# Kernel optimization log

Measured on AMD Instinct MI355X. Metric: run time of the kernel, lower is better.

The kernel has to match this reference:

```python
import jax, jax.numpy as jnp
import numpy as np

N = 8000      # genes (nodes)
P = 32        # pathways (subgraphs, each over all N nodes)
E = 128000    # global edges
ES = 4096     # edges per pathway subgraph
DIN = 16      # in_dim (omics features)
D = 128       # in_dim * 8
K1, K2, K3 = 6400, 5120, 4096  # ceil(0.8*N), ceil(0.8*K1), ceil(0.8*K2)


def setup_inputs() -> dict:
    key = jax.random.key(0)
    ks = jax.random.split(key, 16)
    f = lambda i, shape: jax.random.normal(ks[i], shape, jnp.float32) * 0.05
    edge_index = jax.random.randint(ks[0], (2, E), 0, N, dtype=jnp.int32)
    base = jax.random.randint(ks[1], (2, P, ES), 0, N, dtype=jnp.int32)
    sub_edge_index = (base + (jnp.arange(P, dtype=jnp.int32) * N)[None, :, None]).reshape(2, -1)
    return dict(
        h=jax.random.normal(ks[2], (N, DIN), jnp.float32),
        edge_index=edge_index,
        sub_edge_index=sub_edge_index,
        Wl_a=f(3, (DIN, D)), Wr_a=f(4, (DIN, D)), bl_a=jnp.zeros((D,), jnp.float32),
        # stacked SAGEConv params: [0]=conv_b [1]=conv_c [2]=conv1 [3]=conv2 [4]=conv3
        Wl_s=f(5, (5, D, D)), Wr_s=f(6, (5, D, D)), bl_s=jnp.zeros((5, D), jnp.float32),
        # GlobalAttention gates: [0..2]=readout_a/b/c  [3..5]=readout1/2/3
        gate_w=f(7, (6, D)), gate_b=jnp.zeros((6,), jnp.float32),
        # SAGPooling score GraphConv (D->1): lin_rel (w,b) + lin_root (w)
        pool_wrel=f(8, (3, D)), pool_brel=jnp.zeros((3,), jnp.float32), pool_wroot=f(9, (3, D)),
        norm_w=jnp.ones((D,), jnp.float32), norm_b=jnp.zeros((D,), jnp.float32), norm_ms=jnp.ones((D,), jnp.float32),
        lin_w=f(10, (3 * D, 1)), lin_b=jnp.zeros((1,), jnp.float32),
        m1_w=f(11, (P + 1, 48)), m1_b=jnp.zeros((48,), jnp.float32),
        m2_w=f(12, (48, 16)), m2_b=jnp.zeros((16,), jnp.float32),
        m3_w=f(13, (16, 1)), m3_b=jnp.zeros((1,), jnp.float32),
    )


def _sage(x, src, dst, w, Wl, Wr, bl, n):
    # PyG SAGEConv (aggr='mean'): lin_l(mean_j x_j) + lin_r(x); w = edge live mask
    s = jax.ops.segment_sum(x[src] * w[:, None], dst, num_segments=n)
    deg = jax.ops.segment_sum(w, dst, num_segments=n)
    return (s / jnp.maximum(deg, 1.0)[:, None]) @ Wl + bl + x @ Wr


def _gnorm(x, w, b, ms):
    # PyG GraphNorm, single graph (batch=None)
    mu = x.mean(0)
    o = x - mu * ms
    var = (o * o).mean(0)
    return w * o / jnp.sqrt(var + 1e-5) + b


def reference(h, edge_index, sub_edge_index, Wl_a, Wr_a, bl_a, Wl_s, Wr_s, bl_s,
              gate_w, gate_b, pool_wrel, pool_brel, pool_wroot,
              norm_w, norm_b, norm_ms, lin_w, lin_b,
              m1_w, m1_b, m2_w, m2_b, m3_w, m3_b):
    # ---- stage 1: whole graph, add self loops ----
    loop = jnp.arange(N, dtype=edge_index.dtype)
    src = jnp.concatenate([edge_index[0], loop])
    dst = jnp.concatenate([edge_index[1], loop])
    w1 = jnp.ones(src.shape[0], h.dtype)

    def ro_single(x, i):  # GlobalAttention, batch=None -> one graph
        a = jax.nn.softmax(x @ gate_w[i] + gate_b[i])
        return (a @ x)[None, :]

    x = jnp.tanh(_sage(h, src, dst, w1, Wl_a, Wr_a, bl_a, N))
    x1 = ro_single(x, 0)
    x = _gnorm(x, norm_w, norm_b, norm_ms)
    x = jnp.tanh(_sage(x, src, dst, w1, Wl_s[0], Wr_s[0], bl_s[0], N))
    x2 = ro_single(x, 1)
    x = _gnorm(x, norm_w, norm_b, norm_ms)
    x = jnp.tanh(_sage(x, src, dst, w1, Wl_s[1], Wr_s[1], bl_s[1], N))
    x3 = ro_single(x, 2)
    readout1 = jnp.concatenate([x1, x2, x3], axis=1)  # [1, 3D]

    # ---- stage 2: P pathway subgraphs, each over all N nodes (Data(x=x, edge_index=sub)) ----
    X = jnp.tile(x, (P, 1))            # [P*N, D]
    ssrc, sdst = sub_edge_index[0], sub_edge_index[1]
    ealive = jnp.ones(ssrc.shape, bool)
    nalive = jnp.ones((P, N), bool)

    def sagpool(x, ealive, nalive, i, k):
        # score via GraphConv (aggr='add'); keep top-k per graph; x *= tanh(score)
        w = ealive.astype(x.dtype)
        agg = jax.ops.segment_sum(x[ssrc] * w[:, None], sdst, num_segments=P * N)
        score = agg @ pool_wrel[i] + pool_brel[i] + x @ pool_wroot[i]  # [P*N]
        masked = jnp.where(nalive, score.reshape(P, N), -jnp.inf)
        _, idx = jax.lax.top_k(masked, k)
        na = jnp.zeros((P, N), bool).at[jnp.arange(P)[:, None], idx].set(True)
        xm = jnp.where(na.reshape(-1, 1), x * jnp.tanh(score)[:, None], 0.0)
        naf = na.reshape(-1)
        return xm, ealive & naf[ssrc] & naf[sdst], na

    def ro_batch(x, nalive, i):  # GlobalAttention with batch vector (masked per-graph softmax)
        g = jnp.where(nalive, (x @ gate_w[i] + gate_b[i]).reshape(P, N), -jnp.inf)
        a = jax.nn.softmax(g, axis=1)
        return jnp.einsum('pn,pnd->pd', a, x.reshape(P, N, D))

    x = jnp.tanh(_sage(X, ssrc, sdst, ealive.astype(X.dtype), Wl_s[2], Wr_s[2], bl_s[2], P * N))
    x, ealive, nalive = sagpool(x, ealive, nalive, 0, K1)
    r1 = ro_batch(x, nalive, 3)
    x = jnp.tanh(_sage(x, ssrc, sdst, ealive.astype(x.dtype), Wl_s[3], Wr_s[3], bl_s[3], P * N))
    x, ealive, nalive = sagpool(x, ealive, nalive, 1, K2)
    r2 = ro_batch(x, nalive, 4)
    x = jnp.tanh(_sage(x, ssrc, sdst, ealive.astype(x.dtype), Wl_s[4], Wr_s[4], bl_s[4], P * N))
    x, ealive, nalive = sagpool(x, ealive, nalive, 2, K3)
    r3 = ro_batch(x, nalive, 5)
    readout2 = jnp.concatenate([r1, r2, r3], axis=1)  # [P, 3D]

    ro = jnp.concatenate([readout1, readout2], axis=0)        # [P+1, 3D]
    ro = jnp.tanh((ro @ lin_w + lin_b).T)                     # [1, P+1]
    hid = jnp.tanh(ro @ m1_w + m1_b)                          # dropout inactive at eval
    hid = jnp.tanh(hid @ m2_w + m2_b)
    return jax.nn.sigmoid(jax.nn.sigmoid(hid @ m3_w + m3_b))  # mlp ends in Sigmoid, then outer sigmoid
```

## Files before the change

### kernel.cpp

```cpp
#include <hip/hip_runtime.h>
#include <math.h>

#define NN      8000
#define PP      32
#define EG      128000
#define ES_TOT  131072
#define ES_P    4096
#define PN      256000
#define DI      16
#define DD      128
#define KK1     6400
#define KK2     5120
#define KK3     4096
#define RB      64
#define BPG     (NN / RB)

typedef __attribute__((ext_vector_type(8))) short short8;
typedef __attribute__((ext_vector_type(4))) float f32x4;

static __device__ __forceinline__ unsigned fkey(float f) {
    unsigned u = __float_as_uint(f);
    return (u & 0x80000000u) ? ~u : (u | 0x80000000u);
}
static __device__ __forceinline__ float fkey_inv(unsigned k) {
    unsigned u = (k & 0x80000000u) ? (k & 0x7FFFFFFFu) : ~k;
    return __uint_as_float(u);
}
static __device__ __forceinline__ unsigned short f2bf(float f) {
    unsigned u = __float_as_uint(f);
    u += 0x7FFFu + ((u >> 16) & 1u);
    return (unsigned short)(u >> 16);
}
static __device__ __forceinline__ float bf2f(unsigned short b) {
    return __uint_as_float((unsigned)b << 16);
}
static __device__ __forceinline__ float ftanh(float x) {
    float e = __expf(2.0f * x);
    return 1.0f - 2.0f / (e + 1.0f);
}

__global__ void k_hist(const int* __restrict__ dst, int* __restrict__ cnt, int ne) {
    int e = blockIdx.x * 256 + threadIdx.x;
    if (e < ne) atomicAdd(&cnt[dst[e]], 1);
}

__global__ __launch_bounds__(1024) void k_scanA(const int* __restrict__ cnt,
                                                int* __restrict__ part,
                                                int* __restrict__ bsum, int n) {
    __shared__ int sh[1024];
    int t = threadIdx.x;
    int i = blockIdx.x * 1024 + t;
    int v = (i < n) ? cnt[i] : 0;
    sh[t] = v; __syncthreads();
    for (int off = 1; off < 1024; off <<= 1) {
        int u = (t >= off) ? sh[t - off] : 0;
        __syncthreads();
        sh[t] += u;
        __syncthreads();
    }
    if (i < n) part[i] = sh[t] - v;
    if (t == 1023) bsum[blockIdx.x] = sh[1023];
}

__global__ __launch_bounds__(1024) void k_scanB(int* __restrict__ bsum, int nb) {
    __shared__ int sh[1024];
    int t = threadIdx.x;
    int v = (t < nb) ? bsum[t] : 0;
    sh[t] = v; __syncthreads();
    for (int off = 1; off < 1024; off <<= 1) {
        int u = (t >= off) ? sh[t - off] : 0;
        __syncthreads();
        sh[t] += u;
        __syncthreads();
    }
    if (t < nb) bsum[t] = sh[t] - v;
}

__global__ void k_scanC(const int* __restrict__ part, const int* __restrict__ bsum,
                        int* __restrict__ rowptr, int* __restrict__ cursor, int n, int total) {
    int i = blockIdx.x * 256 + threadIdx.x;
    if (i < n) {
        int v = part[i] + bsum[i >> 10];
        rowptr[i] = v;
        cursor[i] = v;
    }
    if (i == 0) rowptr[n] = total;
}

__global__ void k_scatter(const int* __restrict__ src, const int* __restrict__ dst,
                          int* __restrict__ cursor, int* __restrict__ col, int ne) {
    int e = blockIdx.x * 256 + threadIdx.x;
    if (e >= ne) return;
    int pos = atomicAdd(&cursor[dst[e]], 1);
    col[pos] = src[e];
}

__global__ __launch_bounds__(256) void k_agg16(const float* __restrict__ h,
                                               const int* __restrict__ rowptr,
                                               const int* __restrict__ col,
                                               float* __restrict__ agg, float* __restrict__ deg,
                                               int nrows) {
    int i = blockIdx.x * 256 + threadIdx.x;
    int r = i >> 4, j = i & 15;
    if (r >= nrows) return;
    int b = rowptr[r], e = rowptr[r + 1];
    float a = h[r * 16 + j];
    for (int q = b; q < e; ++q) a += h[col[q] * 16 + j];
    agg[r * 16 + j] = a;
    if (j == 0) deg[r] = 1.0f + (float)(e - b);
}

__global__ __launch_bounds__(256) void k_sage16(
    const float* __restrict__ h, const float* __restrict__ agg, const float* __restrict__ deg,
    const float* __restrict__ Wl, const float* __restrict__ Wr, const float* __restrict__ bl,
    float* __restrict__ y, int nrows)
{
    __shared__ float WlS[16][128], WrS[16][128];
    int tid = threadIdx.x;
    for (int i = tid; i < 16 * 128; i += 256) {
        WlS[i >> 7][i & 127] = Wl[i];
        WrS[i >> 7][i & 127] = Wr[i];
    }
    __syncthreads();
    long long o = (long long)blockIdx.x * 256 + tid;
    int row = (int)(o >> 7);
    if (row >= nrows) return;
    int d = (int)o & 127;
    float invd = 1.0f / fmaxf(deg[row], 1.0f);
    float s = bl[d];
    #pragma unroll
    for (int k = 0; k < 16; ++k)
        s += agg[row * 16 + k] * invd * WlS[k][d] + h[row * 16 + k] * WrS[k][d];
    y[(long long)row * 128 + d] = ftanh(s);
}

__global__ __launch_bounds__(256) void k_aggf0(
    const float* __restrict__ x,
    const int* __restrict__ rowptr, const int* __restrict__ col,
    float* __restrict__ AGG, int nrowsC)
{
    int tid = threadIdx.x;
    int r = blockIdx.x * 8 + (tid >> 5);
    if (r >= nrowsC) return;
    int lane = tid & 31;
    int b = rowptr[r], e = rowptr[r + 1];
    float4 a = *reinterpret_cast<const float4*>(x + (long long)r * 128 + lane * 4);
    float dsum = 1.0f + (float)(e - b);
    for (int q = b; q < e; ++q) {
        int s = col[q];
        float4 v = *reinterpret_cast<const float4*>(x + (long long)s * 128 + lane * 4);
        a.x += v.x; a.y += v.y; a.z += v.z; a.w += v.w;
    }
    float invds = 1.0f / fmaxf(dsum, 1.0f);
    a.x *= invds; a.y *= invds; a.z *= invds; a.w *= invds;
    *reinterpret_cast<float4*>(AGG + (long long)r * 128 + lane * 4) = a;
}

__global__ __launch_bounds__(256) void k_aggf2(
    const unsigned short* __restrict__ x,
    const int* __restrict__ rowptr, const int* __restrict__ col,
    const int* __restrict__ aliveIdx, const float* __restrict__ nal, const float* __restrict__ fvec,
    int rowbase,
    unsigned short* __restrict__ AGGb, int nrowsC)
{
    int tid = threadIdx.x;
    int r = blockIdx.x * 8 + (tid >> 5);
    if (r >= nrowsC) return;
    int lane = tid & 31;
    int orig = aliveIdx[r];
    int grow = rowbase + orig;
    int b = rowptr[grow], e = rowptr[grow + 1];
    float4 a = make_float4(0.0f, 0.0f, 0.0f, 0.0f);
    float dsum = 0.0f;
    for (int q = b; q < e; ++q) {
        int fr = col[q] - rowbase;
        if (nal[fr] == 0.0f) continue;
        dsum += 1.0f;
        float fw = fvec[fr];
        if (fw == 0.0f) continue;
        ushort4 v = *reinterpret_cast<const ushort4*>(x + (long long)fr * 128 + lane * 4);
        a.x += bf2f(v.x) * fw; a.y += bf2f(v.y) * fw;
        a.z += bf2f(v.z) * fw; a.w += bf2f(v.w) * fw;
    }
    float invds = 1.0f / fmaxf(dsum, 1.0f);
    ushort4 o;
    o.x = f2bf(a.x * invds); o.y = f2bf(a.y * invds);
    o.z = f2bf(a.z * invds); o.w = f2bf(a.w * invds);
    *reinterpret_cast<ushort4*>(AGGb + (long long)r * 128 + lane * 4) = o;
}

__global__ __launch_bounds__(256) void k_sage_d(
    const float* __restrict__ AGG, const float* __restrict__ xsrc,
    const float* __restrict__ Wl, const float* __restrict__ Wr, const float* __restrict__ bl,
    float* __restrict__ y, int nrowsC,
    const float* __restrict__ gw, float* __restrict__ gdot)
{
    __shared__ float Ws[32 * 128];
    __shared__ float Is[32][68];
    __shared__ float gwS[128];
    int tid = threadIdx.x;
    long long row0 = (long long)blockIdx.x * 64;
    if (tid < 128 && gw) gwS[tid] = gw[tid];
    __syncthreads();
    int tx = tid & 31, ty = tid >> 5;
    float gg4[4] = {0,0,0,0};
    if (gw) { gg4[0]=gwS[tx*4]; gg4[1]=gwS[tx*4+1]; gg4[2]=gwS[tx*4+2]; gg4[3]=gwS[tx*4+3]; }
    int srow = tid & 63;
    int koff = (tid >> 6) * 8;
    long long crow = row0 + srow;
    if (crow >= nrowsC) crow = nrowsC - 1;
    const float* selfp = xsrc + crow * 128;
    const float* aggp = AGG + crow * 128;

    float acc[8][4] = {};
    for (int kb = 0; kb < 8; ++kb) {
        __syncthreads();
        bool isAgg = (kb < 4);
        const float* Wsrc = isAgg ? (Wl + kb * 32 * 128) : (Wr + (kb - 4) * 32 * 128);
        #pragma unroll
        for (int j = 0; j < 4; ++j) {
            int fl = j * 1024 + tid * 4;
            *reinterpret_cast<float4*>(&Ws[fl]) = *reinterpret_cast<const float4*>(&Wsrc[fl]);
        }
        {
            const float* sp = (isAgg ? (aggp + kb * 32) : (selfp + (kb - 4) * 32)) + koff;
            float4 v0 = *reinterpret_cast<const float4*>(sp);
            float4 v1 = *reinterpret_cast<const float4*>(sp + 4);
            Is[koff + 0][srow] = v0.x; Is[koff + 1][srow] = v0.y;
            Is[koff + 2][srow] = v0.z; Is[koff + 3][srow] = v0.w;
            Is[koff + 4][srow] = v1.x; Is[koff + 5][srow] = v1.y;
            Is[koff + 6][srow] = v1.z; Is[koff + 7][srow] = v1.w;
        }
        __syncthreads();
        #pragma unroll
        for (int kk = 0; kk < 32; ++kk) {
            float4 wv = *reinterpret_cast<const float4*>(&Ws[kk * 128 + tx * 4]);
            float4 i0 = *reinterpret_cast<const float4*>(&Is[kk][ty * 8]);
            float4 i1 = *reinterpret_cast<const float4*>(&Is[kk][ty * 8 + 4]);
            float ia[8] = {i0.x, i0.y, i0.z, i0.w, i1.x, i1.y, i1.z, i1.w};
            float wa[4] = {wv.x, wv.y, wv.z, wv.w};
            #pragma unroll
            for (int i = 0; i < 8; ++i)
                #pragma unroll
                for (int j = 0; j < 4; ++j)
                    acc[i][j] += ia[i] * wa[j];
        }
    }
    float4 bl0 = *reinterpret_cast<const float4*>(&bl[tx * 4]);
    float br[4] = {bl0.x, bl0.y, bl0.z, bl0.w};
    #pragma unroll
    for (int i = 0; i < 8; ++i) {
        long long row = row0 + ty * 8 + i;
        bool valid = (row < nrowsC);
        float yv[4];
        #pragma unroll
        for (int j = 0; j < 4; ++j) yv[j] = ftanh(acc[i][j] + br[j]);
        if (valid)
            *reinterpret_cast<float4*>(&y[row * 128 + tx * 4]) = make_float4(yv[0], yv[1], yv[2], yv[3]);
        float gp = 0.0f;
        #pragma unroll
        for (int j = 0; j < 4; ++j) if (gdot) gp += yv[j] * gg4[j];
        #pragma unroll
        for (int m = 16; m >= 1; m >>= 1) if (gdot) gp += __shfl_xor(gp, m, 32);
        if (tx == 0 && valid && gdot) gdot[row] = gp;
    }
}

__global__ void k_packW(const float* __restrict__ Wl, const float* __restrict__ Wr,
                        short* __restrict__ Wb) {
    int i = blockIdx.x * 256 + threadIdx.x;
    if (i >= 32768) return;
    int kt = i >> 12, rem = i & 4095;
    int ct = rem >> 9; rem &= 511;
    int lane = rem >> 3, e = rem & 7;
    int k = kt * 32 + (lane >> 4) * 8 + e;
    int c = ct * 16 + (lane & 15);
    float v = (k < 128) ? Wl[k * 128 + c] : Wr[(k - 128) * 128 + c];
    Wb[i] = (short)f2bf(v);
}

__global__ __launch_bounds__(256) void k_sage_m(
    const unsigned short* __restrict__ AGGb, const unsigned short* __restrict__ X,
    const int* __restrict__ aliveIdx, const float* __restrict__ fvec,
    const short* __restrict__ Wb, const float* __restrict__ bl,
    unsigned short* __restrict__ y, int nrowsC,
    const float* __restrict__ wrel, const float* __restrict__ wroot, const float* __restrict__ gw,
    float* __restrict__ tbuf, float* __restrict__ rootd, float* __restrict__ gdot)
{
    __shared__ short8 lB[2048];
    int tid = threadIdx.x;
    int lane = tid & 63;
    int wv = tid >> 6;
    long long rows0 = (long long)blockIdx.x * 64 + wv * 16;
    int arow = lane & 15;
    int ksl = (lane >> 4) * 8;

    int growA = (int)(rows0 + arow);
    int origA = aliveIdx[growA];
    float fsA = fvec[origA];

    f32x4 acc[8] = {};
    const short8* Wbv = (const short8*)Wb;

    for (int half = 0; half < 2; ++half) {
        __syncthreads();
        #pragma unroll
        for (int i = 0; i < 8; ++i) {
            int idx = i * 256 + tid;
            lB[idx] = Wbv[half * 2048 + idx];
        }
        __syncthreads();
        #pragma unroll
        for (int ktl = 0; ktl < 4; ++ktl) {
            int kt = half * 4 + ktl;
            short8 afr;
            if (kt < 4) {
                afr = *reinterpret_cast<const short8*>(AGGb + (long long)growA * 128 + kt * 32 + ksl);
            } else {
                short8 xv = *reinterpret_cast<const short8*>(X + (long long)origA * 128 + (kt - 4) * 32 + ksl);
                #pragma unroll
                for (int e = 0; e < 8; ++e)
                    afr[e] = (short)f2bf(bf2f((unsigned short)xv[e]) * fsA);
            }
            #pragma unroll
            for (int ct = 0; ct < 8; ++ct) {
                short8 bfr = lB[(ktl * 8 + ct) * 64 + lane];
                acc[ct] = __builtin_amdgcn_mfma_f32_16x16x32_bf16(afr, bfr, acc[ct], 0, 0, 0);
            }
        }
    }

    int ocol = lane & 15;
    float blv[8], wrv[8], wov[8], ggv[8];
    #pragma unroll
    for (int ct = 0; ct < 8; ++ct) {
        int c = ct * 16 + ocol;
        blv[ct] = bl[c];
        wrv[ct] = wrel[c];
        wov[ct] = wroot[c];
        ggv[ct] = gw[c];
    }
    #pragma unroll
    for (int j = 0; j < 4; ++j) {
        int rloc = (lane >> 4) * 4 + j;
        long long grow = rows0 + rloc;
        int orig = aliveIdx[grow];
        float tp = 0.0f, rp = 0.0f, gp = 0.0f;
        #pragma unroll
        for (int ct = 0; ct < 8; ++ct) {
            float v = ftanh(acc[ct][j] + blv[ct]);
            y[(long long)orig * 128 + ct * 16 + ocol] = f2bf(v);
            tp += v * wrv[ct]; rp += v * wov[ct]; gp += v * ggv[ct];
        }
        #pragma unroll
        for (int mm = 8; mm >= 1; mm >>= 1) {
            tp += __shfl_xor(tp, mm, 16);
            rp += __shfl_xor(rp, mm, 16);
            gp += __shfl_xor(gp, mm, 16);
        }
        if (ocol == 0) { tbuf[orig] = tp; rootd[orig] = rp; gdot[orig] = gp; }
    }
}

__global__ __launch_bounds__(256) void k_gemm_self(
    const float* __restrict__ x, const float* __restrict__ W, const float* __restrict__ b,
    float* __restrict__ y, int nrows)
{
    __shared__ float Ws[32 * 128];
    __shared__ float Is[32][68];
    int tid = threadIdx.x;
    long long row0 = (long long)blockIdx.x * 64;
    int tx = tid & 31, ty = tid >> 5;
    int srow = tid & 63;
    int koff = (tid >> 6) * 8;
    long long lrow = row0 + srow;
    if (lrow >= nrows) lrow = nrows - 1;
    const float* xrow = x + lrow * 128;
    float acc[8][4] = {};
    for (int kb = 0; kb < 4; ++kb) {
        __syncthreads();
        const float* Wsrc = W + kb * 32 * 128;
        #pragma unroll
        for (int j = 0; j < 4; ++j) {
            int fl = j * 1024 + tid * 4;
            *reinterpret_cast<float4*>(&Ws[fl]) = *reinterpret_cast<const float4*>(&Wsrc[fl]);
        }
        {
            const float* sp = xrow + kb * 32 + koff;
            float4 v0 = *reinterpret_cast<const float4*>(sp);
            float4 v1 = *reinterpret_cast<const float4*>(sp + 4);
            Is[koff + 0][srow] = v0.x; Is[koff + 1][srow] = v0.y;
            Is[koff + 2][srow] = v0.z; Is[koff + 3][srow] = v0.w;
            Is[koff + 4][srow] = v1.x; Is[koff + 5][srow] = v1.y;
            Is[koff + 6][srow] = v1.z; Is[koff + 7][srow] = v1.w;
        }
        __syncthreads();
        #pragma unroll
        for (int kk = 0; kk < 32; ++kk) {
            float4 wv = *reinterpret_cast<const float4*>(&Ws[kk * 128 + tx * 4]);
            float4 i0 = *reinterpret_cast<const float4*>(&Is[kk][ty * 8]);
            float4 i1 = *reinterpret_cast<const float4*>(&Is[kk][ty * 8 + 4]);
            float ia[8] = {i0.x, i0.y, i0.z, i0.w, i1.x, i1.y, i1.z, i1.w};
            float wa[4] = {wv.x, wv.y, wv.z, wv.w};
            #pragma unroll
            for (int i = 0; i < 8; ++i)
                #pragma unroll
                for (int j = 0; j < 4; ++j)
                    acc[i][j] += ia[i] * wa[j];
        }
    }
    float4 b0 = b ? *reinterpret_cast<const float4*>(&b[tx * 4]) : make_float4(0.f, 0.f, 0.f, 0.f);
    #pragma unroll
    for (int i = 0; i < 8; ++i) {
        long long row = row0 + ty * 8 + i;
        if (row >= nrows) continue;
        *reinterpret_cast<float4*>(&y[row * 128 + tx * 4]) =
            make_float4(acc[i][0] + b0.x, acc[i][1] + b0.y, acc[i][2] + b0.z, acc[i][3] + b0.w);
    }
}

__global__ __launch_bounds__(256) void k_l0comb(
    const float* __restrict__ ZL0, const float* __restrict__ zself,
    const int* __restrict__ rowptr, const int* __restrict__ col, int rowbase,
    const float* __restrict__ wrel, const float* __restrict__ wroot, const float* __restrict__ gw,
    unsigned short* __restrict__ y, float* __restrict__ tbuf, float* __restrict__ rootd, float* __restrict__ gdot,
    int nrowsC)
{
    __shared__ float wrelS[128], wrootS[128], gwS[128];
    int tid = threadIdx.x;
    if (tid < 128) {
        wrelS[tid]  = wrel[tid];
        wrootS[tid] = wroot[tid];
        gwS[tid]    = gw[tid];
    }
    __syncthreads();
    int r = blockIdx.x * 8 + (tid >> 5);
    if (r >= nrowsC) return;
    int lane = tid & 31;
    int grow = rowbase + r;
    int b = rowptr[grow], e = rowptr[grow + 1];
    float4 a = make_float4(0.0f, 0.0f, 0.0f, 0.0f);
    for (int q = b; q < e; ++q) {
        int fr = col[q] % NN;
        float4 v = *reinterpret_cast<const float4*>(ZL0 + (long long)fr * 128 + lane * 4);
        a.x += v.x; a.y += v.y; a.z += v.z; a.w += v.w;
    }
    float invds = 1.0f / fmaxf((float)(e - b), 1.0f);
    const float4 z = *reinterpret_cast<const float4*>(zself + (long long)(r % NN) * 128 + lane * 4);
    float yv[4];
    yv[0] = ftanh(a.x * invds + z.x);
    yv[1] = ftanh(a.y * invds + z.y);
    yv[2] = ftanh(a.z * invds + z.z);
    yv[3] = ftanh(a.w * invds + z.w);
    ushort4 o;
    o.x = f2bf(yv[0]); o.y = f2bf(yv[1]); o.z = f2bf(yv[2]); o.w = f2bf(yv[3]);
    *reinterpret_cast<ushort4*>(y + (long long)r * 128 + lane * 4) = o;
    float tp = 0.0f, rp = 0.0f, gp = 0.0f;
    #pragma unroll
    for (int j = 0; j < 4; ++j) {
        tp += yv[j] * wrelS[lane*4 + j];
        rp += yv[j] * wrootS[lane*4 + j];
        gp += yv[j] * gwS[lane*4 + j];
    }
    #pragma unroll
    for (int m = 16; m >= 1; m >>= 1) {
        tp += __shfl_xor(tp, m, 32);
        rp += __shfl_xor(rp, m, 32);
        gp += __shfl_xor(gp, m, 32);
    }
    if (lane == 0) {
        tbuf[r]  = tp;
        rootd[r] = rp;
        gdot[r]  = gp;
    }
}

__global__ __launch_bounds__(256) void k_gate(
    const float* __restrict__ X, const float* __restrict__ gw,
    float* __restrict__ g, int nrows)
{
    __shared__ float wS[128];
    if (threadIdx.x < 128) wS[threadIdx.x] = gw[threadIdx.x];
    __syncthreads();
    int i = blockIdx.x * 256 + threadIdx.x;
    if (i >= nrows) return;
    const float4* xrp = reinterpret_cast<const float4*>(X + (long long)i * 128);
    float s = 0.0f;
    #pragma unroll
    for (int k = 0; k < 32; ++k) {
        float4 v = xrp[k];
        s += v.x * wS[4*k] + v.y * wS[4*k+1] + v.z * wS[4*k+2] + v.w * wS[4*k+3];
    }
    g[i] = s;
}

__global__ __launch_bounds__(1024) void k_smstats(float* __restrict__ g, float* __restrict__ invp) {
    __shared__ float red[1024];
    int p = blockIdx.x, tid = threadIdx.x;
    float* gp = g + (long long)p * NN;
    float lmax = -INFINITY;
    for (int n = tid; n < NN; n += 1024) lmax = fmaxf(lmax, gp[n]);
    red[tid] = lmax; __syncthreads();
    for (int s = 512; s > 0; s >>= 1) { if (tid < s) red[tid] = fmaxf(red[tid], red[tid + s]); __syncthreads(); }
    float mx = red[0]; __syncthreads();
    float ls = 0.0f;
    for (int n = tid; n < NN; n += 1024) { float e = __expf(gp[n] - mx); gp[n] = e; ls += e; }
    red[tid] = ls; __syncthreads();
    for (int s = 512; s > 0; s >>= 1) { if (tid < s) red[tid] += red[tid + s]; __syncthreads(); }
    if (tid == 0) invp[p] = 1.0f / red[0];
}

__global__ __launch_bounds__(128) void k_wsum(
    const float* __restrict__ X, const float* __restrict__ a,
    const float* __restrict__ invp, float* __restrict__ ro, int rowbase, int colOff)
{
    int p = blockIdx.x / BPG;
    int chunk = blockIdx.x % BPG;
    int d = threadIdx.x;
    long long base = (long long)p * NN;
    int r0 = chunk * RB, r1 = r0 + RB;
    float s = 0.0f;
    for (int n = r0; n < r1; ++n) {
        float w = a[base + n];
        if (w != 0.0f) s += w * X[(base + n) * 128 + d];
    }
    atomicAdd(&ro[(long long)(rowbase + p) * 384 + colOff + d], s * invp[p]);
}

__global__ __launch_bounds__(128) void k_wsum_c(
    const unsigned short* __restrict__ X, const float* __restrict__ gbuf, const float* __restrict__ fvec,
    const float* __restrict__ invp, const int* __restrict__ aliveIdx, int k,
    float* __restrict__ ro, int rowbaseRo, int colOff)
{
    int bpp = k / RB;
    int p = blockIdx.x / bpp;
    int chunk = blockIdx.x % bpp;
    int d = threadIdx.x;
    const int* ai = aliveIdx + (long long)p * k + chunk * RB;
    float s = 0.0f;
    for (int j = 0; j < RB; ++j) {
        int row = ai[j];
        float w = gbuf[row] * fvec[row];
        s += w * bf2f(X[(long long)row * 128 + d]);
    }
    atomicAdd(&ro[(long long)(rowbaseRo + p) * 384 + colOff + d], s * invp[p]);
}

__global__ void k_colstat(const float* __restrict__ x, float* __restrict__ musum,
                          float* __restrict__ sqsum, int nrows) {
    int d = threadIdx.x;
    int r0 = blockIdx.x * 64;
    int r1 = min(r0 + 64, nrows);
    float s = 0.0f, q = 0.0f;
    for (int r = r0; r < r1; ++r) { float v = x[(long long)r * 128 + d]; s += v; q += v * v; }
    atomicAdd(&musum[d], s);
    atomicAdd(&sqsum[d], q);
}

__global__ void k_gnorm_apply(const float* __restrict__ x, float* __restrict__ y,
                              const float* __restrict__ musum, const float* __restrict__ sqsum,
                              const float* __restrict__ w, const float* __restrict__ b,
                              const float* __restrict__ ms, int nrows) {
    long long i = (long long)blockIdx.x * 256 + threadIdx.x;
    if (i >= (long long)nrows * 128) return;
    int d = (int)(i & 127);
    float inv_n = 1.0f / (float)nrows;
    float mu = musum[d] * inv_n;
    float c = mu * ms[d];
    float var = sqsum[d] * inv_n - 2.0f * c * mu + c * c;
    y[i] = w[d] * (x[i] - c) * rsqrtf(var + 1e-5f) + b[d];
}

#define TCH 8
__global__ __launch_bounds__(1024) void k_topk2(
    const int* __restrict__ rowptr, const int* __restrict__ col, int rowbase,
    const float* __restrict__ tb, const float* __restrict__ rootd,
    const float* __restrict__ gdot, const float* __restrict__ brelp, int bi, int allAlive,
    float* __restrict__ nalive, float* __restrict__ fvec, float* __restrict__ gbuf,
    float* __restrict__ invp, int* __restrict__ aliveIdx, int k)
{
    __shared__ unsigned keys[NN];
    __shared__ int hist[256];
    __shared__ int scan[1024];
    __shared__ float redf[1024];
    __shared__ unsigned sh_pref;
    __shared__ int sh_kneed;
    int p = blockIdx.x, tid = threadIdx.x;
    float brel = brelp[bi];
    long long pbase = (long long)p * NN;
    for (int n = tid; n < NN; n += 1024) {
        long long gl = pbase + n;
        int grow = rowbase + (int)gl;
        float s = brel + rootd[gl];
        int b = rowptr[grow], e = rowptr[grow + 1];
        for (int q = b; q < e; ++q) {
            int sl = col[q] - rowbase;
            s += allAlive ? tb[sl] : (tb[sl] * nalive[sl]);
        }
        bool alive = allAlive || (nalive[gl] > 0.5f);
        keys[n] = alive ? fkey(s) : 0u;
    }
    if (tid == 0) { sh_pref = 0u; sh_kneed = k; }
    __syncthreads();
    for (int lvl = 3; lvl >= 0; --lvl) {
        int sh = lvl * 8;
        if (tid < 256) hist[tid] = 0;
        unsigned pref = sh_pref; int kneed = sh_kneed;
        unsigned pmask = (lvl == 3) ? 0u : (0xFFFFFFFFu << (8 * (lvl + 1)));
        __syncthreads();
        for (int n = tid; n < NN; n += 1024) {
            unsigned kv = keys[n];
            if ((kv & pmask) == pref) atomicAdd(&hist[(kv >> sh) & 255], 1);
        }
        __syncthreads();
        if (tid < 256) scan[tid] = hist[tid];
        __syncthreads();
        for (int off = 1; off < 256; off <<= 1) {
            int v = 0;
            if (tid < 256 && tid + off < 256) v = scan[tid + off];
            __syncthreads();
            if (tid < 256) scan[tid] += v;
            __syncthreads();
        }
        if (tid < 256) {
            int c = scan[tid];
            int cex = c - hist[tid];
            if (c >= kneed && cex < kneed) {
                sh_pref = pref | ((unsigned)tid << sh);
                sh_kneed = kneed - cex;
            }
        }
        __syncthreads();
    }
    unsigned V = sh_pref;
    int seleq = sh_kneed;
    int c0 = tid * TCH, c1 = min(c0 + TCH, NN);
    int ceq = 0;
    for (int n = c0; n < c1; ++n) ceq += (keys[n] == V) ? 1 : 0;
    scan[tid] = ceq; __syncthreads();
    for (int off = 1; off < 1024; off <<= 1) {
        int u = (tid >= off) ? scan[tid - off] : 0;
        __syncthreads();
        scan[tid] += u;
        __syncthreads();
    }
    int rank = scan[tid] - ceq;
    unsigned selmask = 0u;
    int nsel = 0;
    float lmax = -INFINITY;
    for (int n = c0; n < c1; ++n) {
        unsigned kk = keys[n];
        bool sel = (kk > V) || (kk == V && rank < seleq);
        if (kk == V) rank++;
        long long gl = pbase + n;
        nalive[gl] = sel ? 1.0f : 0.0f;
        float f = 0.0f;
        if (sel) {
            f = ftanh(fkey_inv(kk));
            lmax = fmaxf(lmax, f * gdot[gl]);
            selmask |= (1u << (n - c0));
            ++nsel;
        }
        fvec[gl] = f;
    }
    redf[tid] = lmax; __syncthreads();
    for (int s = 512; s > 0; s >>= 1) { if (tid < s) redf[tid] = fmaxf(redf[tid], redf[tid + s]); __syncthreads(); }
    float mx = redf[0]; __syncthreads();
    scan[tid] = nsel; __syncthreads();
    for (int off = 1; off < 1024; off <<= 1) {
        int u = (tid >= off) ? scan[tid - off] : 0;
        __syncthreads();
        scan[tid] += u;
        __syncthreads();
    }
    int pos = scan[tid] - nsel;
    float lsum = 0.0f;
    for (int n = c0; n < c1; ++n) {
        if (selmask & (1u << (n - c0))) {
            long long gl = pbase + n;
            float e = __expf(fvec[gl] * gdot[gl] - mx);
            gbuf[gl] = e;
            lsum += e;
            aliveIdx[(long long)p * k + pos] = (int)gl;
            ++pos;
        }
    }
    redf[tid] = lsum; __syncthreads();
    for (int s = 512; s > 0; s >>= 1) { if (tid < s) redf[tid] += redf[tid + s]; __syncthreads(); }
    if (tid == 0) invp[p] = 1.0f / redf[0];
}

__global__ __launch_bounds__(64) void k_head(
    const float* __restrict__ ro, const float* __restrict__ lin_w, const float* __restrict__ lin_b,
    const float* __restrict__ m1w, const float* __restrict__ m1b,
    const float* __restrict__ m2w, const float* __restrict__ m2b,
    const float* __restrict__ m3w, const float* __restrict__ m3b, float* __restrict__ out)
{
    __shared__ float v[33], h1[48], h2[16];
    int t = threadIdx.x;
    if (t < 33) {
        float s = lin_b[0];
        for (int k = 0; k < 384; ++k) s += ro[t * 384 + k] * lin_w[k];
        v[t] = tanhf(s);
    }
    __syncthreads();
    if (t < 48) {
        float s = m1b[t];
        for (int i = 0; i < 33; ++i) s += v[i] * m1w[i * 48 + t];
        h1[t] = tanhf(s);
    }
    __syncthreads();
    if (t < 16) {
        float s = m2b[t];
        for (int i = 0; i < 48; ++i) s += h1[i] * m2w[i * 16 + t];
        h2[t] = tanhf(s);
    }
    __syncthreads();
    if (t == 0) {
        float s = m3b[0];
        for (int i = 0; i < 16; ++i) s += h2[i] * m3w[i];
        float s1 = 1.0f / (1.0f + expf(-s));
        out[0] = 1.0f / (1.0f + expf(-s1));
    }
}

static inline int cdiv(long long a, long long b) { return (int)((a + b - 1) / b); }

extern "C" void kernel_launch(void* const* d_in, const int* in_sizes, int n_in,
                              void* d_out, int out_size, void* d_ws, size_t ws_size,
                              hipStream_t stream)
{
    (void)in_sizes; (void)n_in; (void)out_size;
    const float* h     = (const float*)d_in[0];
    const int*   eidx  = (const int*)d_in[1];
    const int*   seidx = (const int*)d_in[2];
    const float* Wl_a  = (const float*)d_in[3];
    const float* Wr_a  = (const float*)d_in[4];
    const float* bl_a  = (const float*)d_in[5];
    const float* Wl_s  = (const float*)d_in[6];
    const float* Wr_s  = (const float*)d_in[7];
    const float* bl_s  = (const float*)d_in[8];
    const float* gate_w = (const float*)d_in[9];
    const float* p_wrel = (const float*)d_in[11];
    const float* p_brel = (const float*)d_in[12];
    const float* p_wroot= (const float*)d_in[13];
    const float* nw    = (const float*)d_in[14];
    const float* nb    = (const float*)d_in[15];
    const float* nms   = (const float*)d_in[16];
    const float* lin_w = (const float*)d_in[17];
    const float* lin_b = (const float*)d_in[18];
    const float* m1w   = (const float*)d_in[19];
    const float* m1b   = (const float*)d_in[20];
    const float* m2w   = (const float*)d_in[21];
    const float* m2b   = (const float*)d_in[22];
    const float* m3w   = (const float*)d_in[23];
    const float* m3b   = (const float*)d_in[24];
    float* out = (float*)d_out;

    const int* esrc = eidx;
    const int* edst = eidx + EG;
    const int* ssrc = seidx;
    const int* sdst = seidx + ES_TOT;

    auto need_bytes = [](int chp) -> size_t {
        long long chn = (long long)chp * NN;
        long long f = chn * 64
                    + (long long)chp * KK1 * 64
                    + 2LL * NN * 128
                    + 5 * chn
                    + 64 + 33 * 384
                    + (long long)chp * KK1
                    + (PN + 1) + ES_TOT
                    + 2 * 16384
                    + 64 * 24;
        return (size_t)f * 4;
    };
    int chp = 8;
    if (ws_size >= need_bytes(32)) chp = 32;
    else if (ws_size >= need_bytes(16)) chp = 16;
    int nch = PP / chp;
    long long ch_n = (long long)chp * NN;

    float* W = (float*)d_ws;
    size_t off = 0;
    auto alloc = [&](size_t nf) { float* p = W + off; off += (nf + 63) & ~(size_t)63; return p; };
    unsigned short* XAb = (unsigned short*)alloc((size_t)ch_n * 64);
    unsigned short* AGGb = (unsigned short*)alloc((size_t)chp * KK1 * 64);
    float* ZL0   = alloc((size_t)NN * DD);
    float* zself = alloc((size_t)NN * DD);
    float* tbuf  = alloc(ch_n);
    float* rootd = alloc(ch_n);
    float* nal   = alloc(ch_n);
    float* fvec  = alloc(ch_n);
    float* gdot  = alloc(ch_n);
    float* invp  = alloc(64);
    float* ro    = alloc(33 * 384);
    int* aliveIdx = (int*)alloc((size_t)chp * KK1);
    int* s2rp    = (int*)alloc(PN + 1);
    int* s2col   = (int*)alloc(ES_TOT);
    short* Wb1   = (short*)alloc(16384);
    short* Wb2   = (short*)alloc(16384);
    float* gbuf = tbuf;

    float* XO = (float*)XAb;
    size_t ooff = 0;
    auto oalloc = [&](size_t nf) { float* p = XO + ooff; ooff += (nf + 63) & ~(size_t)63; return p; };
    float* xa    = oalloc((size_t)NN * DD);
    float* xb    = oalloc((size_t)NN * DD);
    float* AGGs  = oalloc((size_t)NN * DD);
    float* agg1  = oalloc((size_t)NN * 16);
    float* deg1  = oalloc(NN);
    float* musum = oalloc(128);
    float* sqsum = oalloc(128);
    int* s1cnt  = (int*)oalloc(NN);
    int* s1rp   = (int*)oalloc(NN + 1);
    int* s1cur  = (int*)oalloc(NN);
    int* s1col  = (int*)oalloc(EG);
    int* s1part = (int*)oalloc(NN);
    int* s1bsum = (int*)oalloc(1024);
    int* s2cnt  = (int*)oalloc(PN);
    int* s2cur  = (int*)oalloc(PN);
    int* s2part = (int*)oalloc(PN);
    int* s2bsum = (int*)oalloc(1024);

    int nb1 = cdiv(NN, 1024), nb2 = cdiv(PN, 1024);
    hipMemsetAsync(s1cnt, 0, NN * sizeof(int), stream);
    k_hist<<<cdiv(EG,256),256,0,stream>>>(edst, s1cnt, EG);
    k_scanA<<<nb1,1024,0,stream>>>(s1cnt, s1part, s1bsum, NN);
    k_scanB<<<1,1024,0,stream>>>(s1bsum, nb1);
    k_scanC<<<cdiv(NN,256),256,0,stream>>>(s1part, s1bsum, s1rp, s1cur, NN, EG);
    k_scatter<<<cdiv(EG,256),256,0,stream>>>(esrc, edst, s1cur, s1col, EG);

    hipMemsetAsync(s2cnt, 0, (size_t)PN * sizeof(int), stream);
    k_hist<<<cdiv(ES_TOT,256),256,0,stream>>>(sdst, s2cnt, ES_TOT);
    k_scanA<<<nb2,1024,0,stream>>>(s2cnt, s2part, s2bsum, PN);
    k_scanB<<<1,1024,0,stream>>>(s2bsum, nb2);
    k_scanC<<<cdiv(PN,256),256,0,stream>>>(s2part, s2bsum, s2rp, s2cur, PN, ES_TOT);
    k_scatter<<<cdiv(ES_TOT,256),256,0,stream>>>(ssrc, sdst, s2cur, s2col, ES_TOT);

    hipMemsetAsync(ro, 0, 33 * 384 * sizeof(float), stream);

    k_packW<<<128,256,0,stream>>>(Wl_s + 3*16384, Wr_s + 3*16384, Wb1);
    k_packW<<<128,256,0,stream>>>(Wl_s + 4*16384, Wr_s + 4*16384, Wb2);

    k_agg16<<<cdiv((long long)NN*16,256),256,0,stream>>>(h, s1rp, s1col, agg1, deg1, NN);
    k_sage16<<<cdiv((long long)NN*DD,256),256,0,stream>>>(h, agg1, deg1, Wl_a, Wr_a, bl_a, xa, NN);
    k_gate<<<cdiv(NN,256),256,0,stream>>>(xa, gate_w + 0*DD, gbuf, NN);
    k_smstats<<<1,1024,0,stream>>>(gbuf, invp);
    k_wsum<<<BPG,128,0,stream>>>(xa, gbuf, invp, ro, 0, 0);

    hipMemsetAsync(musum, 0, 128*sizeof(float), stream);
    hipMemsetAsync(sqsum, 0, 128*sizeof(float), stream);
    k_colstat<<<cdiv(NN,64),128,0,stream>>>(xa, musum, sqsum, NN);
    k_gnorm_apply<<<cdiv((long long)NN*DD,256),256,0,stream>>>(xa, xb, musum, sqsum, nw, nb, nms, NN);

    k_aggf0<<<cdiv(NN,8),256,0,stream>>>(xb, s1rp, s1col, AGGs, NN);
    k_sage_d<<<cdiv(NN,64),256,0,stream>>>(AGGs, xb,
        Wl_s + 0*16384, Wr_s + 0*16384, bl_s + 0*128, xa, NN,
        gate_w + 1*DD, gbuf);
    k_smstats<<<1,1024,0,stream>>>(gbuf, invp);
    k_wsum<<<BPG,128,0,stream>>>(xa, gbuf, invp, ro, 0, 128);

    hipMemsetAsync(musum, 0, 128*sizeof(float), stream);
    hipMemsetAsync(sqsum, 0, 128*sizeof(float), stream);
    k_colstat<<<cdiv(NN,64),128,0,stream>>>(xa, musum, sqsum, NN);
    k_gnorm_apply<<<cdiv((long long)NN*DD,256),256,0,stream>>>(xa, xb, musum, sqsum, nw, nb, nms, NN);

    k_aggf0<<<cdiv(NN,8),256,0,stream>>>(xb, s1rp, s1col, AGGs, NN);
    k_sage_d<<<cdiv(NN,64),256,0,stream>>>(AGGs, xb,
        Wl_s + 1*16384, Wr_s + 1*16384, bl_s + 1*128, xa, NN,
        gate_w + 2*DD, gbuf);
    k_smstats<<<1,1024,0,stream>>>(gbuf, invp);
    k_wsum<<<BPG,128,0,stream>>>(xa, gbuf, invp, ro, 0, 256);

    k_gemm_self<<<cdiv(NN,64),256,0,stream>>>(xa, Wl_s + 2*16384, nullptr, ZL0, NN);
    k_gemm_self<<<cdiv(NN,64),256,0,stream>>>(xa, Wr_s + 2*16384, bl_s + 2*128, zself, NN);

    for (int c = 0; c < nch; ++c) {
        int nbase = (int)(c * ch_n);

        k_l0comb<<<(int)(ch_n/8),256,0,stream>>>(ZL0, zself, s2rp, s2col, nbase,
            p_wrel + 0*DD, p_wroot + 0*DD, gate_w + 3*DD,
            XAb, tbuf, rootd, gdot, (int)ch_n);
        k_topk2<<<chp,1024,0,stream>>>(s2rp, s2col, nbase, tbuf, rootd, gdot, p_brel, 0, 1,
                                       nal, fvec, gbuf, invp, aliveIdx, KK1);
        k_wsum_c<<<chp*(KK1/RB),128,0,stream>>>(XAb, gbuf, fvec, invp, aliveIdx, KK1, ro, 1 + c*chp, 0);

        k_aggf2<<<chp*(KK1/8),256,0,stream>>>(XAb, s2rp, s2col, aliveIdx, nal, fvec, nbase, AGGb, chp*KK1);
        k_sage_m<<<chp*(KK1/64),256,0,stream>>>(AGGb, XAb, aliveIdx, fvec, Wb1, bl_s + 3*128, XAb, chp*KK1,
            p_wrel + 1*DD, p_wroot + 1*DD, gate_w + 4*DD, tbuf, rootd, gdot);
        k_topk2<<<chp,1024,0,stream>>>(s2rp, s2col, nbase, tbuf, rootd, gdot, p_brel, 1, 0,
                                       nal, fvec, gbuf, invp, aliveIdx, KK2);
        k_wsum_c<<<chp*(KK2/RB),128,0,stream>>>(XAb, gbuf, fvec, invp, aliveIdx, KK2, ro, 1 + c*chp, 128);

        k_aggf2<<<chp*(KK2/8),256,0,stream>>>(XAb, s2rp, s2col, aliveIdx, nal, fvec, nbase, AGGb, chp*KK2);
        k_sage_m<<<chp*(KK2/64),256,0,stream>>>(AGGb, XAb, aliveIdx, fvec, Wb2, bl_s + 4*128, XAb, chp*KK2,
            p_wrel + 2*DD, p_wroot + 2*DD, gate_w + 5*DD, tbuf, rootd, gdot);
        k_topk2<<<chp,1024,0,stream>>>(s2rp, s2col, nbase, tbuf, rootd, gdot, p_brel, 2, 0,
                                       nal, fvec, gbuf, invp, aliveIdx, KK3);
        k_wsum_c<<<chp*(KK3/RB),128,0,stream>>>(XAb, gbuf, fvec, invp, aliveIdx, KK3, ro, 1 + c*chp, 256);
    }

    k_head<<<1,64,0,stream>>>(ro, lin_w, lin_b, m1w, m1b, m2w, m2b, m3w, m3b, out);
}
```

Before: 703.3 us.

## Split top-k scoring into grid-wide kernel and use wave-shuffle scans in selection

The per-node score computation (CSR gather over neighbour scores) moves out of the single-block-per-pathway top-k kernel into a separate kernel that spreads over many blocks and writes sort keys to global memory. The top-k kernel then loads those keys into shared memory with vector loads. It also replaces its shared-memory Hillis-Steele scans and tree reductions, which need many barriers, with wavefront shuffle scans and reductions plus a small cross-wave step. This is meant to fix the low parallelism of running only chp blocks for the irregular gather and to cut barrier count, at the cost of an extra launch and a global round trip for the keys.

```diff
diff --git a/kernel.cpp b/kernel.cpp
--- a/kernel.cpp
+++ b/kernel.cpp
@@ -571,37 +571,45 @@
     y[i] = w[d] * (x[i] - c) * rsqrtf(var + 1e-5f) + b[d];
 }
 
-#define TCH 8
-__global__ __launch_bounds__(1024) void k_topk2(
+__global__ __launch_bounds__(256) void k_score2(
     const int* __restrict__ rowptr, const int* __restrict__ col, int rowbase,
     const float* __restrict__ tb, const float* __restrict__ rootd,
-    const float* __restrict__ gdot, const float* __restrict__ brelp, int bi, int allAlive,
+    const float* __restrict__ brelp, int bi, int allAlive,
+    const float* __restrict__ nalive, unsigned* __restrict__ keysG, int n)
+{
+    int r = blockIdx.x * 256 + threadIdx.x;
+    if (r >= n) return;
+    int grow = rowbase + r;
+    float s = brelp[bi] + rootd[r];
+    int b = rowptr[grow], e = rowptr[grow + 1];
+    for (int q = b; q < e; ++q) {
+        int sl = col[q] - rowbase;
+        s += allAlive ? tb[sl] : (tb[sl] * nalive[sl]);
+    }
+    bool alive = allAlive || (nalive[r] > 0.5f);
+    keysG[r] = alive ? fkey(s) : 0u;
+}
+
+__global__ __launch_bounds__(1024) void k_topk3(
+    const unsigned* __restrict__ keysG, const float* __restrict__ gdot,
     float* __restrict__ nalive, float* __restrict__ fvec, float* __restrict__ gbuf,
     float* __restrict__ invp, int* __restrict__ aliveIdx, int k)
 {
     __shared__ unsigned keys[NN];
     __shared__ int hist[256];
-    __shared__ int scan[1024];
-    __shared__ float redf[1024];
+    __shared__ int wred[16];
+    __shared__ float wredf[16];
     __shared__ unsigned sh_pref;
     __shared__ int sh_kneed;
     int p = blockIdx.x, tid = threadIdx.x;
-    float brel = brelp[bi];
+    int lane = tid & 63, wid = tid >> 6;
     long long pbase = (long long)p * NN;
-    for (int n = tid; n < NN; n += 1024) {
-        long long gl = pbase + n;
-        int grow = rowbase + (int)gl;
-        float s = brel + rootd[gl];
-        int b = rowptr[grow], e = rowptr[grow + 1];
-        for (int q = b; q < e; ++q) {
-            int sl = col[q] - rowbase;
-            s += allAlive ? tb[sl] : (tb[sl] * nalive[sl]);
-        }
-        bool alive = allAlive || (nalive[gl] > 0.5f);
-        keys[n] = alive ? fkey(s) : 0u;
-    }
+    const uint4* kg = reinterpret_cast<const uint4*>(keysG + pbase);
+    for (int i = tid; i < NN / 4; i += 1024)
+        *reinterpret_cast<uint4*>(&keys[i * 4]) = kg[i];
     if (tid == 0) { sh_pref = 0u; sh_kneed = k; }
     __syncthreads();
+
     for (int lvl = 3; lvl >= 0; --lvl) {
         int sh = lvl * 8;
         if (tid < 256) hist[tid] = 0;
@@ -613,42 +621,62 @@
             if ((kv & pmask) == pref) atomicAdd(&hist[(kv >> sh) & 255], 1);
         }
         __syncthreads();
-        if (tid < 256) scan[tid] = hist[tid];
-        __syncthreads();
-        for (int off = 1; off < 256; off <<= 1) {
-            int v = 0;
-            if (tid < 256 && tid + off < 256) v = scan[tid + off];
-            __syncthreads();
-            if (tid < 256) scan[tid] += v;
-            __syncthreads();
-        }
-        if (tid < 256) {
-            int c = scan[tid];
-            int cex = c - hist[tid];
-            if (c >= kneed && cex < kneed) {
-                sh_pref = pref | ((unsigned)tid << sh);
-                sh_kneed = kneed - cex;
+        if (wid == 0) {
+            int b0 = 252 - 4 * lane;
+            int h0 = hist[b0], h1 = hist[b0 + 1], h2 = hist[b0 + 2], h3 = hist[b0 + 3];
+            int s3 = h3, s2 = h2 + s3, s1 = h1 + s2, s0 = h0 + s1;
+            int gs = s0;
+            #pragma unroll
+            for (int d = 1; d < 64; d <<= 1) {
+                int u = __shfl_up(gs, d, 64);
+                if (lane >= d) gs += u;
             }
-        }
-        __syncthreads();
-    }
+            int above = gs - s0;
+            int suf0 = above + s0, suf1 = above + s1, suf2 = above + s2, suf3 = above + s3;
+            if (suf0 >= kneed && suf0 - h0 < kneed) { sh_pref = pref | ((unsigned)b0 << sh); sh_kneed = kneed - (suf0 - h0); }
+            if (suf1 >= kneed && suf1 - h1 < kneed) { sh_pref = pref | ((unsigned)(b0+1) << sh); sh_kneed = kneed - (suf1 - h1); }
+            if (suf2 >= kneed && suf2 - h2 < kneed) { sh_pref = pref | ((unsigned)(b0+2) << sh); sh_kneed = kneed - (suf2 - h2); }
+            if (suf3 >= kneed && suf3 - h3 < kneed) { sh_pref = pref | ((unsigned)(b0+3) << sh); sh_kneed = kneed - (suf3 - h3); }
+        }
+        __syncthreads();
+    }
+
     unsigned V = sh_pref;
     int seleq = sh_kneed;
-    int c0 = tid * TCH, c1 = min(c0 + TCH, NN);
+    int c0 = tid * 8;
     int ceq = 0;
-    for (int n = c0; n < c1; ++n) ceq += (keys[n] == V) ? 1 : 0;
-    scan[tid] = ceq; __syncthreads();
-    for (int off = 1; off < 1024; off <<= 1) {
-        int u = (tid >= off) ? scan[tid - off] : 0;
-        __syncthreads();
-        scan[tid] += u;
-        __syncthreads();
-    }
-    int rank = scan[tid] - ceq;
+    #pragma unroll
+    for (int j = 0; j < 8; ++j) {
+        int n = c0 + j;
+        if (n < NN) ceq += (keys[n] == V) ? 1 : 0;
+    }
+    int vv = ceq;
+    #pragma unroll
+    for (int d = 1; d < 64; d <<= 1) {
+        int u = __shfl_up(vv, d, 64);
+        if (lane >= d) vv += u;
+    }
+    if (lane == 63) wred[wid] = vv;
+    __syncthreads();
+    if (tid < 16) {
+        int w = wred[tid];
+        #pragma unroll
+        for (int d = 1; d < 16; d <<= 1) {
+            int u = __shfl_up(w, d, 16);
+            if (tid >= d) w += u;
+        }
+        wred[tid] = w;
+    }
+    __syncthreads();
+    int rank = vv - ceq + (wid > 0 ? wred[wid - 1] : 0);
+
     unsigned selmask = 0u;
     int nsel = 0;
     float lmax = -INFINITY;
-    for (int n = c0; n < c1; ++n) {
+    #pragma unroll
+    for (int j = 0; j < 8; ++j) {
+        int n = c0 + j;
+        if (n >= NN) break;
         unsigned kk = keys[n];
         bool sel = (kk > V) || (kk == V && rank < seleq);
         if (kk == V) rank++;
@@ -658,25 +686,49 @@
         if (sel) {
             f = ftanh(fkey_inv(kk));
             lmax = fmaxf(lmax, f * gdot[gl]);
-            selmask |= (1u << (n - c0));
+            selmask |= (1u << j);
             ++nsel;
         }
         fvec[gl] = f;
     }
-    redf[tid] = lmax; __syncthreads();
-    for (int s = 512; s > 0; s >>= 1) { if (tid < s) redf[tid] = fmaxf(redf[tid], redf[tid + s]); __syncthreads(); }
-    float mx = redf[0]; __syncthreads();
-    scan[tid] = nsel; __syncthreads();
-    for (int off = 1; off < 1024; off <<= 1) {
-        int u = (tid >= off) ? scan[tid - off] : 0;
-        __syncthreads();
-        scan[tid] += u;
-        __syncthreads();
-    }
-    int pos = scan[tid] - nsel;
+    #pragma unroll
+    for (int d = 32; d >= 1; d >>= 1) lmax = fmaxf(lmax, __shfl_xor(lmax, d, 64));
+    if (lane == 0) wredf[wid] = lmax;
+    __syncthreads();
+    if (tid < 16) {
+        float m = wredf[tid];
+        #pragma unroll
+        for (int d = 8; d >= 1; d >>= 1) m = fmaxf(m, __shfl_xor(m, d, 16));
+        if (tid == 0) wredf[0] = m;
+    }
+    __syncthreads();
+    float mx = wredf[0];
+    __syncthreads();
+    int v2 = nsel;
+    #pragma unroll
+    for (int d = 1; d < 64; d <<= 1) {
+        int u = __shfl_up(v2, d, 64);
+        if (lane >= d) v2 += u;
+    }
+    if (lane == 63) wred[wid] = v2;
+    __syncthreads();
+    if (tid < 16) {
+        int w = wred[tid];
+        #pragma unroll
+        for (int d = 1; d < 16; d <<= 1) {
+            int u = __shfl_up(w, d, 16);
+            if (tid >= d) w += u;
+        }
+        wred[tid] = w;
+    }
+    __syncthreads();
+    int pos = v2 - nsel + (wid > 0 ? wred[wid - 1] : 0);
+
     float lsum = 0.0f;
-    for (int n = c0; n < c1; ++n) {
-        if (selmask & (1u << (n - c0))) {
+    #pragma unroll
+    for (int j = 0; j < 8; ++j) {
+        if (selmask & (1u << j)) {
+            int n = c0 + j;
             long long gl = pbase + n;
             float e = __expf(fvec[gl] * gdot[gl] - mx);
             gbuf[gl] = e;
@@ -685,9 +737,16 @@
             ++pos;
         }
     }
-    redf[tid] = lsum; __syncthreads();
-    for (int s = 512; s > 0; s >>= 1) { if (tid < s) redf[tid] += redf[tid + s]; __syncthreads(); }
-    if (tid == 0) invp[p] = 1.0f / redf[0];
+    #pragma unroll
+    for (int d = 32; d >= 1; d >>= 1) lsum += __shfl_xor(lsum, d, 64);
+    if (lane == 0) wredf[wid] = lsum;
+    __syncthreads();
+    if (tid < 16) {
+        float s = wredf[tid];
+        #pragma unroll
+        for (int d = 8; d >= 1; d >>= 1) s += __shfl_xor(s, d, 16);
+        if (tid == 0) invp[p] = 1.0f / s;
+    }
 }
 
 __global__ __launch_bounds__(64) void k_head(
@@ -768,11 +827,12 @@
                     + (long long)chp * KK1 * 64
                     + 2LL * NN * 128
                     + 5 * chn
+                    + chn
                     + 64 + 33 * 384
                     + (long long)chp * KK1
                     + (PN + 1) + ES_TOT
                     + 2 * 16384
-                    + 64 * 24;
+                    + 64 * 28;
         return (size_t)f * 4;
     };
     int chp = 8;
@@ -793,6 +853,7 @@
     float* nal   = alloc(ch_n);
     float* fvec  = alloc(ch_n);
     float* gdot  = alloc(ch_n);
+    unsigned* keysG = (unsigned*)alloc(ch_n);
     float* invp  = alloc(64);
     float* ro    = alloc(33 * 384);
     int* aliveIdx = (int*)alloc((size_t)chp * KK1);
@@ -882,22 +943,25 @@
         k_l0comb<<<(int)(ch_n/8),256,0,stream>>>(ZL0, zself, s2rp, s2col, nbase,
             p_wrel + 0*DD, p_wroot + 0*DD, gate_w + 3*DD,
             XAb, tbuf, rootd, gdot, (int)ch_n);
-        k_topk2<<<chp,1024,0,stream>>>(s2rp, s2col, nbase, tbuf, rootd, gdot, p_brel, 0, 1,
-                                       nal, fvec, gbuf, invp, aliveIdx, KK1);
+        k_score2<<<(int)(ch_n/256),256,0,stream>>>(s2rp, s2col, nbase, tbuf, rootd, p_brel, 0, 1,
+                                                   nal, keysG, (int)ch_n);
+        k_topk3<<<chp,1024,0,stream>>>(keysG, gdot, nal, fvec, gbuf, invp, aliveIdx, KK1);
         k_wsum_c<<<chp*(KK1/RB),128,0,stream>>>(XAb, gbuf, fvec, invp, aliveIdx, KK1, ro, 1 + c*chp, 0);
 
         k_aggf2<<<chp*(KK1/8),256,0,stream>>>(XAb, s2rp, s2col, aliveIdx, nal, fvec, nbase, AGGb, chp*KK1);
         k_sage_m<<<chp*(KK1/64),256,0,stream>>>(AGGb, XAb, aliveIdx, fvec, Wb1, bl_s + 3*128, XAb, chp*KK1,
             p_wrel + 1*DD, p_wroot + 1*DD, gate_w + 4*DD, tbuf, rootd, gdot);
-        k_topk2<<<chp,1024,0,stream>>>(s2rp, s2col, nbase, tbuf, rootd, gdot, p_brel, 1, 0,
-                                       nal, fvec, gbuf, invp, aliveIdx, KK2);
+        k_score2<<<(int)(ch_n/256),256,0,stream>>>(s2rp, s2col, nbase, tbuf, rootd, p_brel, 1, 0,
+                                                   nal, keysG, (int)ch_n);
+        k_topk3<<<chp,1024,0,stream>>>(keysG, gdot, nal, fvec, gbuf, invp, aliveIdx, KK2);
         k_wsum_c<<<chp*(KK2/RB),128,0,stream>>>(XAb, gbuf, fvec, invp, aliveIdx, KK2, ro, 1 + c*chp, 128);
 
         k_aggf2<<<chp*(KK2/8),256,0,stream>>>(XAb, s2rp, s2col, aliveIdx, nal, fvec, nbase, AGGb, chp*KK2);
         k_sage_m<<<chp*(KK2/64),256,0,stream>>>(AGGb, XAb, aliveIdx, fvec, Wb2, bl_s + 4*128, XAb, chp*KK2,
             p_wrel + 2*DD, p_wroot + 2*DD, gate_w + 5*DD, tbuf, rootd, gdot);
-        k_topk2<<<chp,1024,0,stream>>>(s2rp, s2col, nbase, tbuf, rootd, gdot, p_brel, 2, 0,
-                                       nal, fvec, gbuf, invp, aliveIdx, KK3);
+        k_score2<<<(int)(ch_n/256),256,0,stream>>>(s2rp, s2col, nbase, tbuf, rootd, p_brel, 2, 0,
+                                                   nal, keysG, (int)ch_n);
+        k_topk3<<<chp,1024,0,stream>>>(keysG, gdot, nal, fvec, gbuf, invp, aliveIdx, KK3);
         k_wsum_c<<<chp*(KK3/RB),128,0,stream>>>(XAb, gbuf, fvec, invp, aliveIdx, KK3, ro, 1 + c*chp, 256);
     }
 
```

After: 657.1 us. -6.6%, faster.
